# Kernel tuning notes

Hardware: AMD Instinct MI355X
Metric: run time of the kernel (lower is better)

Reference implementation:

```python
import jax, jax.numpy as jnp
import numpy as np
from jax import lax

N_PTS = 256          # hardcoded point count in original loops
BIG = 257.0 ** 2     # initial SE sentinel in original code


def setup_inputs() -> dict:
    key = jax.random.key(0)
    k1, k2 = jax.random.split(key)
    B = 2048
    inp = jax.random.normal(k1, (B, 1, 2 * N_PTS), dtype=jnp.float32)
    tgt = jax.random.normal(k2, (B, 1, 2 * N_PTS), dtype=jnp.float32)
    return {"input": inp, "targets": tgt}


def reference(input, targets):
    B = input.shape[0]
    # interleaved (x, y) pairs -> [B, 256, 2]
    pin = input[:, 0, :].reshape(B, N_PTS, 2)
    ptg = targets[:, 0, :].reshape(B, N_PTS, 2)
    # pairwise squared distances: D[b, j, k] = ||tgt_j - in_k||^2
    D = jnp.sum((ptg[:, :, None, :] - pin[:, None, :, :]) ** 2, axis=-1)  # [B,256,256]
    big = jnp.asarray(BIG, dtype=D.dtype)
    batch_idx = jnp.arange(B)

    def step(used, dj):
        # dj: [B, 256] distances from target point j to all input points
        vals = jnp.where(used, jnp.inf, dj)
        m = jnp.min(vals, axis=1)
        k = jnp.argmin(vals, axis=1)
        se = jnp.minimum(m, big)              # SE stays 257^2 if nothing beats it
        k = jnp.where(m < big, k, 0)          # k_tmp stays 0 in that case
        used = used.at[batch_idx, k].set(True)
        return used, se

    used0 = jnp.zeros((B, N_PTS), dtype=bool)
    _, ses = lax.scan(step, used0, jnp.swapaxes(D, 0, 1))  # iterate j=0..255, ses: [256, B]
    loss = jnp.sum(ses) / B / (2 * N_PTS)
    return loss
```

## Files before the change

### kernel.cpp

```cpp
#include <hip/hip_runtime.h>
#include <stdint.h>

#define N_PTS 256
#define BIG_F 66049.0f

template<int CTRL, int ROW_MASK, int BANK_MASK>
__device__ __forceinline__ float dpp_min_f32(float x) {
    int xi = __float_as_int(x);
    int yi = __builtin_amdgcn_update_dpp(xi, xi, CTRL, ROW_MASK, BANK_MASK, false);
    return fminf(x, __int_as_float(yi));
}

__device__ __forceinline__ float wave_reduce_min_bcast(float x) {
    x = dpp_min_f32<0x111, 0xf, 0xf>(x);
    x = dpp_min_f32<0x112, 0xf, 0xf>(x);
    x = dpp_min_f32<0x114, 0xf, 0xf>(x);
    x = dpp_min_f32<0x118, 0xf, 0xf>(x);
    x = dpp_min_f32<0x142, 0xa, 0xf>(x);
    x = dpp_min_f32<0x143, 0xc, 0xf>(x);
    return __int_as_float(__builtin_amdgcn_readlane(__float_as_int(x), 63));
}

__device__ __forceinline__ void greedy_phase(
    float txc, float tyc, int lane, float& acc,
    float& px0, float& py0, float& px1, float& py1,
    float& px2, float& py2, float& px3, float& py3)
{
    #pragma clang fp contract(off)
    const float NANF = __int_as_float(0x7fc00000);
    #pragma unroll 1
    for (int j2 = 0; j2 < 64; ++j2) {
        float tjx = __int_as_float(__builtin_amdgcn_readlane(__float_as_int(txc), j2));
        float tjy = __int_as_float(__builtin_amdgcn_readlane(__float_as_int(tyc), j2));

        float dx0 = tjx - px0, dy0 = tjy - py0;
        float dx1 = tjx - px1, dy1 = tjy - py1;
        float dx2 = tjx - px2, dy2 = tjy - py2;
        float dx3 = tjx - px3, dy3 = tjy - py3;
        float d0 = dx0 * dx0 + dy0 * dy0;
        float d1 = dx1 * dx1 + dy1 * dy1;
        float d2 = dx2 * dx2 + dy2 * dy2;
        float d3 = dx3 * dx3 + dy3 * dy3;

        float m = fminf(fminf(d0, d1), fminf(d2, d3));
        m = wave_reduce_min_bcast(m);

        unsigned long long e0 = __ballot(d0 == m);
        unsigned long long e1 = __ballot(d1 == m);
        unsigned long long e2 = __ballot(d2 == m);
        unsigned long long e3 = __ballot(d3 == m);
        int k = e0 ? (__ffsll((long long)e0) - 1)
              : e1 ? (64  + __ffsll((long long)e1) - 1)
              : e2 ? (128 + __ffsll((long long)e2) - 1)
              :      (192 + __ffsll((long long)e3) - 1);

        bool ok = (m < BIG_F);
        m = ok ? m : BIG_F;
        k = ok ? k : 0;

        acc += m;

        const int  ks  = k >> 6;
        const bool hit = (lane == (k & 63));
        px0 = (hit && ks == 0) ? NANF : px0;
        px1 = (hit && ks == 1) ? NANF : px1;
        px2 = (hit && ks == 2) ? NANF : px2;
        px3 = (hit && ks == 3) ? NANF : px3;
    }
}

__global__ __launch_bounds__(256) void greedy_match_kernel(
    const float* __restrict__ input,
    const float* __restrict__ targets,
    float* __restrict__ out,
    int B, float scale)
{
    __shared__ float wsum[4];
    const int lane = threadIdx.x & 63;
    const int wid  = threadIdx.x >> 6;
    const int b    = blockIdx.x * 4 + wid;

    float acc = 0.0f;
    if (b < B) {
        const float2* pin = (const float2*)(input   + (size_t)b * (2 * N_PTS));
        const float2* ptg = (const float2*)(targets + (size_t)b * (2 * N_PTS));

        float2 p0 = pin[lane],       t0 = ptg[lane];
        float2 p1 = pin[64 + lane],  t1 = ptg[64 + lane];
        float2 p2 = pin[128 + lane], t2 = ptg[128 + lane];
        float2 p3 = pin[192 + lane], t3 = ptg[192 + lane];

        float px0 = p0.x, py0 = p0.y, px1 = p1.x, py1 = p1.y;
        float px2 = p2.x, py2 = p2.y, px3 = p3.x, py3 = p3.y;

        greedy_phase(t0.x, t0.y, lane, acc, px0, py0, px1, py1, px2, py2, px3, py3);
        greedy_phase(t1.x, t1.y, lane, acc, px0, py0, px1, py1, px2, py2, px3, py3);
        greedy_phase(t2.x, t2.y, lane, acc, px0, py0, px1, py1, px2, py2, px3, py3);
        greedy_phase(t3.x, t3.y, lane, acc, px0, py0, px1, py1, px2, py2, px3, py3);
    }

    if (lane == 0) wsum[wid] = acc;
    __syncthreads();
    if (threadIdx.x == 0) {
        float s = (wsum[0] + wsum[1] + wsum[2] + wsum[3]) * scale;
        atomicAdd(out, s);
    }
}

extern "C" void kernel_launch(void* const* d_in, const int* in_sizes, int n_in,
                              void* d_out, int out_size, void* d_ws, size_t ws_size,
                              hipStream_t stream) {
    const float* input   = (const float*)d_in[0];
    const float* targets = (const float*)d_in[1];
    float* out = (float*)d_out;

    const int B = in_sizes[0] / (2 * N_PTS);
    const float scale = 1.0f / ((float)B * (float)(2 * N_PTS));

    hipMemsetAsync(d_out, 0, sizeof(float) * (size_t)out_size, stream);

    const int blocks = (B + 3) / 4;
    greedy_match_kernel<<<blocks, 256, 0, stream>>>(input, targets, out, B, scale);
}
```

Before: 128.3 us.

## Process two greedy steps speculatively per iteration with conflict fallback

Each loop iteration now computes distances and wave-wide minima for two consecutive target points at once, interleaving their DPP reductions and ballots to expose instruction-level parallelism across the serial greedy chain. The second point's result is used unless it picked the same input point as the first. On a collision it recomputes against the updated (poisoned) set. This halves the dependent-latency steps in the common case, at the cost of extra ALU work and a divergent-free but occasional serial fallback.

```diff
diff --git a/kernel.cpp b/kernel.cpp
--- a/kernel.cpp
+++ b/kernel.cpp
@@ -4,68 +4,126 @@
 #define N_PTS 256
 #define BIG_F 66049.0f
 
-template<int CTRL, int ROW_MASK, int BANK_MASK>
-__device__ __forceinline__ float dpp_min_f32(float x) {
+typedef unsigned long long ull;
+
+template<int CTRL>
+__device__ __forceinline__ float dpp_min1(float x) {
     int xi = __float_as_int(x);
-    int yi = __builtin_amdgcn_update_dpp(xi, xi, CTRL, ROW_MASK, BANK_MASK, false);
+    int yi = __builtin_amdgcn_update_dpp(xi, xi, CTRL, 0xf, 0xf, false);
     return fminf(x, __int_as_float(yi));
 }
 
-__device__ __forceinline__ float wave_reduce_min_bcast(float x) {
-    x = dpp_min_f32<0x111, 0xf, 0xf>(x);
-    x = dpp_min_f32<0x112, 0xf, 0xf>(x);
-    x = dpp_min_f32<0x114, 0xf, 0xf>(x);
-    x = dpp_min_f32<0x118, 0xf, 0xf>(x);
-    x = dpp_min_f32<0x142, 0xa, 0xf>(x);
-    x = dpp_min_f32<0x143, 0xc, 0xf>(x);
-    return __int_as_float(__builtin_amdgcn_readlane(__float_as_int(x), 63));
+__device__ __forceinline__ void wave_min2(float& a, float& b) {
+    a = dpp_min1<0x111>(a); b = dpp_min1<0x111>(b);
+    a = dpp_min1<0x112>(a); b = dpp_min1<0x112>(b);
+    a = dpp_min1<0x114>(a); b = dpp_min1<0x114>(b);
+    a = dpp_min1<0x118>(a); b = dpp_min1<0x118>(b);
+    a = dpp_min1<0x142>(a); b = dpp_min1<0x142>(b);
+    a = dpp_min1<0x143>(a); b = dpp_min1<0x143>(b);
+    a = __int_as_float(__builtin_amdgcn_readlane(__float_as_int(a), 63));
+    b = __int_as_float(__builtin_amdgcn_readlane(__float_as_int(b), 63));
 }
 
-__device__ __forceinline__ void greedy_phase(
+__device__ __forceinline__ float wave_min1(float a) {
+    a = dpp_min1<0x111>(a);
+    a = dpp_min1<0x112>(a);
+    a = dpp_min1<0x114>(a);
+    a = dpp_min1<0x118>(a);
+    a = dpp_min1<0x142>(a);
+    a = dpp_min1<0x143>(a);
+    return __int_as_float(__builtin_amdgcn_readlane(__float_as_int(a), 63));
+}
+
+__device__ __forceinline__ int pick_k(ull e0, ull e1, ull e2, ull e3) {
+    return e0 ? (__ffsll((long long)e0) - 1)
+         : e1 ? (64  + __ffsll((long long)e1) - 1)
+         : e2 ? (128 + __ffsll((long long)e2) - 1)
+         :      (192 + __ffsll((long long)e3) - 1);
+}
+
+__device__ __forceinline__ void poison(int k, int lane,
+    float& px0, float& px1, float& px2, float& px3) {
+    const float NANF = __int_as_float(0x7fc00000);
+    const int  ks  = k >> 6;
+    const bool hit = (lane == (k & 63));
+    px0 = (hit && ks == 0) ? NANF : px0;
+    px1 = (hit && ks == 1) ? NANF : px1;
+    px2 = (hit && ks == 2) ? NANF : px2;
+    px3 = (hit && ks == 3) ? NANF : px3;
+}
+
+__device__ __forceinline__ void greedy_phase_pair(
     float txc, float tyc, int lane, float& acc,
     float& px0, float& py0, float& px1, float& py1,
     float& px2, float& py2, float& px3, float& py3)
 {
     #pragma clang fp contract(off)
-    const float NANF = __int_as_float(0x7fc00000);
     #pragma unroll 1
-    for (int j2 = 0; j2 < 64; ++j2) {
-        float tjx = __int_as_float(__builtin_amdgcn_readlane(__float_as_int(txc), j2));
-        float tjy = __int_as_float(__builtin_amdgcn_readlane(__float_as_int(tyc), j2));
+    for (int j2 = 0; j2 < 64; j2 += 2) {
+        float tAx = __int_as_float(__builtin_amdgcn_readlane(__float_as_int(txc), j2));
+        float tAy = __int_as_float(__builtin_amdgcn_readlane(__float_as_int(tyc), j2));
+        float tBx = __int_as_float(__builtin_amdgcn_readlane(__float_as_int(txc), j2 + 1));
+        float tBy = __int_as_float(__builtin_amdgcn_readlane(__float_as_int(tyc), j2 + 1));
 
-        float dx0 = tjx - px0, dy0 = tjy - py0;
-        float dx1 = tjx - px1, dy1 = tjy - py1;
-        float dx2 = tjx - px2, dy2 = tjy - py2;
-        float dx3 = tjx - px3, dy3 = tjy - py3;
-        float d0 = dx0 * dx0 + dy0 * dy0;
-        float d1 = dx1 * dx1 + dy1 * dy1;
-        float d2 = dx2 * dx2 + dy2 * dy2;
-        float d3 = dx3 * dx3 + dy3 * dy3;
+        float ax0 = tAx - px0, ay0 = tAy - py0;
+        float ax1 = tAx - px1, ay1 = tAy - py1;
+        float ax2 = tAx - px2, ay2 = tAy - py2;
+        float ax3 = tAx - px3, ay3 = tAy - py3;
+        float dA0 = ax0 * ax0 + ay0 * ay0;
+        float dA1 = ax1 * ax1 + ay1 * ay1;
+        float dA2 = ax2 * ax2 + ay2 * ay2;
+        float dA3 = ax3 * ax3 + ay3 * ay3;
+        float bx0 = tBx - px0, by0 = tBy - py0;
+        float bx1 = tBx - px1, by1 = tBy - py1;
+        float bx2 = tBx - px2, by2 = tBy - py2;
+        float bx3 = tBx - px3, by3 = tBy - py3;
+        float dB0 = bx0 * bx0 + by0 * by0;
+        float dB1 = bx1 * bx1 + by1 * by1;
+        float dB2 = bx2 * bx2 + by2 * by2;
+        float dB3 = bx3 * bx3 + by3 * by3;
 
-        float m = fminf(fminf(d0, d1), fminf(d2, d3));
-        m = wave_reduce_min_bcast(m);
+        float mA = fminf(fminf(dA0, dA1), fminf(dA2, dA3));
+        float mB = fminf(fminf(dB0, dB1), fminf(dB2, dB3));
+        wave_min2(mA, mB);
 
-        unsigned long long e0 = __ballot(d0 == m);
-        unsigned long long e1 = __ballot(d1 == m);
-        unsigned long long e2 = __ballot(d2 == m);
-        unsigned long long e3 = __ballot(d3 == m);
-        int k = e0 ? (__ffsll((long long)e0) - 1)
-              : e1 ? (64  + __ffsll((long long)e1) - 1)
-              : e2 ? (128 + __ffsll((long long)e2) - 1)
-              :      (192 + __ffsll((long long)e3) - 1);
+        ull eA0 = __ballot(dA0 == mA);
+        ull eA1 = __ballot(dA1 == mA);
+        ull eA2 = __ballot(dA2 == mA);
+        ull eA3 = __ballot(dA3 == mA);
+        ull eB0 = __ballot(dB0 == mB);
+        ull eB1 = __ballot(dB1 == mB);
+        ull eB2 = __ballot(dB2 == mB);
+        ull eB3 = __ballot(dB3 == mB);
 
-        bool ok = (m < BIG_F);
-        m = ok ? m : BIG_F;
-        k = ok ? k : 0;
+        int kA = pick_k(eA0, eA1, eA2, eA3);
+        bool okA = (mA < BIG_F);
+        acc += okA ? mA : BIG_F;
+        kA = okA ? kA : 0;
+        poison(kA, lane, px0, px1, px2, px3);
 
-        acc += m;
-
-        const int  ks  = k >> 6;
-        const bool hit = (lane == (k & 63));
-        px0 = (hit && ks == 0) ? NANF : px0;
-        px1 = (hit && ks == 1) ? NANF : px1;
-        px2 = (hit && ks == 2) ? NANF : px2;
-        px3 = (hit && ks == 3) ? NANF : px3;
+        int kB = pick_k(eB0, eB1, eB2, eB3);
+        if (kB == kA) {
+            float rx0 = tBx - px0, ry0 = tBy - py0;
+            float rx1 = tBx - px1, ry1 = tBy - py1;
+            float rx2 = tBx - px2, ry2 = tBy - py2;
+            float rx3 = tBx - px3, ry3 = tBy - py3;
+            float r0 = rx0 * rx0 + ry0 * ry0;
+            float r1 = rx1 * rx1 + ry1 * ry1;
+            float r2 = rx2 * rx2 + ry2 * ry2;
+            float r3 = rx3 * rx3 + ry3 * ry3;
+            float m2 = fminf(fminf(r0, r1), fminf(r2, r3));
+            m2 = wave_min1(m2);
+            ull f0 = __ballot(r0 == m2);
+            ull f1 = __ballot(r1 == m2);
+            ull f2 = __ballot(r2 == m2);
+            ull f3 = __ballot(r3 == m2);
+            kB = pick_k(f0, f1, f2, f3);
+            mB = m2;
+        }
+        bool okB = (mB < BIG_F);
+        acc += okB ? mB : BIG_F;
+        kB = okB ? kB : 0;
+        poison(kB, lane, px0, px1, px2, px3);
     }
 }
 
@@ -93,10 +151,10 @@
         float px0 = p0.x, py0 = p0.y, px1 = p1.x, py1 = p1.y;
         float px2 = p2.x, py2 = p2.y, px3 = p3.x, py3 = p3.y;
 
-        greedy_phase(t0.x, t0.y, lane, acc, px0, py0, px1, py1, px2, py2, px3, py3);
-        greedy_phase(t1.x, t1.y, lane, acc, px0, py0, px1, py1, px2, py2, px3, py3);
-        greedy_phase(t2.x, t2.y, lane, acc, px0, py0, px1, py1, px2, py2, px3, py3);
-        greedy_phase(t3.x, t3.y, lane, acc, px0, py0, px1, py1, px2, py2, px3, py3);
+        greedy_phase_pair(t0.x, t0.y, lane, acc, px0, py0, px1, py1, px2, py2, px3, py3);
+        greedy_phase_pair(t1.x, t1.y, lane, acc, px0, py0, px1, py1, px2, py2, px3, py3);
+        greedy_phase_pair(t2.x, t2.y, lane, acc, px0, py0, px1, py1, px2, py2, px3, py3);
+        greedy_phase_pair(t3.x, t3.y, lane, acc, px0, py0, px1, py1, px2, py2, px3, py3);
     }
 
     if (lane == 0) wsum[wid] = acc;
```

After: 128.4 us. About the same (+0.1%).
